# Kernel tuning notes

Measured on AMD Instinct MI355X. Metric: run time of the kernel, lower is better.

Reference implementation:

```python
import math
import jax, jax.numpy as jnp
import numpy as np

H, W = 24, 24
N = H * W
D = 1024
B = 32
MAX_ITERS = 6

# 9 relative neighbor offsets (3x3 window, row-major)
_REL = np.array([[-1, -1], [-1, 0], [-1, 1], [0, -1], [0, 0], [0, 1], [1, -1], [1, 0], [1, 1]])


def _neighbor_cols():
    y, x = np.meshgrid(np.arange(H), np.arange(W), indexing='ij')
    ny = np.clip(y[None] + _REL[:, 0, None, None], 0, H - 1)  # [9,H,W]
    nx = np.clip(x[None] + _REL[:, 1, None, None], 0, W - 1)
    return jnp.asarray((ny * W + nx).reshape(9, N))  # [9,N]


def setup_inputs() -> dict:
    key = jax.random.key(0)
    ks = jax.random.split(key, 8)
    return {
        'tok2d': jax.random.normal(ks[0], (B, N + 1, D), dtype=jnp.float32),
        'dw_w': jax.random.normal(ks[1], (D, 1, 3, 3), dtype=jnp.float32) * 0.02,
        'pw_w': jax.random.normal(ks[2], (9, D, 1, 1), dtype=jnp.float32) * 0.02,
        'pw_b': jnp.zeros((9,), dtype=jnp.float32),
        'q_w': jax.random.normal(ks[3], (D, D), dtype=jnp.float32) * 0.02,
        'q_b': jax.random.normal(ks[4], (D,), dtype=jnp.float32) * 0.02,
        'v_w': jax.random.normal(ks[5], (D, D), dtype=jnp.float32) * 0.02,
        'v_b': jax.random.normal(ks[6], (D,), dtype=jnp.float32) * 0.02,
        'K': 256,
        'MAX_TOKENS': 128,
    }


def _affinity_head(patch2d, dw_w, pw_w, pw_b):
    # patch2d: [B,H,W,D] -> Q: [B,H,W,9]
    x = jnp.transpose(patch2d, (0, 3, 1, 2))  # NCHW
    x = jax.lax.conv_general_dilated(
        x, dw_w, window_strides=(1, 1), padding='SAME',
        feature_group_count=D,
        dimension_numbers=('NCHW', 'OIHW', 'NCHW'))
    x = jnp.einsum('bdhw,od->bohw', x, pw_w[:, :, 0, 0]) + pw_b[None, :, None, None]
    return jax.nn.softmax(jnp.transpose(x, (0, 2, 3, 1)), axis=-1)


def _build_token_affinity(Q):
    # Q: [B,H,W,9] -> A: [B,N,N] via 9 shifted-neighbor scatters
    cols = _neighbor_cols()                                   # [9,N]
    rows = jnp.broadcast_to(jnp.arange(N)[None, :], (9, N))   # [9,N]
    vals = jnp.moveaxis(Q.reshape(-1, N, 9), -1, 1).reshape(-1, 9 * N)  # [B,9*N]
    A = jnp.zeros((Q.shape[0], N, N), dtype=Q.dtype)
    return A.at[:, rows.reshape(-1), cols.reshape(-1)].add(vals)


def _cluster_roots(A):
    roots = jnp.argmax(A, axis=-1)  # [B,N]
    for _ in range(MAX_ITERS):      # pointer jumping (idempotent once converged)
        roots = jnp.take_along_axis(roots, roots, axis=1)
    return roots


def _cluster_centers(E, roots, K):
    b = E.shape[0]
    bidx = jnp.arange(b)[:, None]
    centers_sum = jnp.zeros_like(E).at[bidx, roots].add(E)          # [B,N,D]
    counts = jnp.zeros(E.shape[:2], E.dtype).at[bidx, roots].add(1.0)  # [B,N]
    _, topk_idx = jax.lax.top_k(counts, K)
    ord_idx = jnp.sort(topk_idx, axis=1)
    cs = jnp.take_along_axis(centers_sum, ord_idx[:, :, None], axis=1)
    cnt = jnp.take_along_axis(counts, ord_idx, axis=1)
    C = cs / jnp.clip(cnt, 1.0, None)[:, :, None]
    return C, cnt


def reference(tok2d, dw_w, pw_w, pw_b, q_w, q_b, v_w, v_b, K, MAX_TOKENS):
    cls_tok = tok2d[:, :1, :]                 # [B,1,D]
    patch = tok2d[:, 1:, :]                   # [B,N,D]
    Q = _affinity_head(patch.reshape(-1, H, W, D), dw_w, pw_w, pw_b)
    A = _build_token_affinity(Q)
    roots = _cluster_roots(A)
    C, cnt = _cluster_centers(patch, roots, K)
    Q_cls = cls_tok @ q_w.T + q_b             # [B,1,D]
    K_v = C @ v_w.T + v_b                     # [B,K,D]
    scores = jnp.einsum('bod,bkd->bk', Q_cls, K_v) / math.sqrt(D)
    valid = jnp.where(cnt > 0, scores, -jnp.inf)
    m = min(MAX_TOKENS, C.shape[1])
    _, idx = jax.lax.top_k(valid, m)
    idx_sorted = jnp.sort(idx, axis=-1)
    return jnp.take_along_axis(C, idx_sorted[:, :, None], axis=1)  # [B,m,D]
```

## Files before the change

kernel.cpp:

```cpp
#include <hip/hip_runtime.h>
#include <math.h>

#define Hh 24
#define Ww 24
#define Nn 576
#define Dd 1024
#define Bb 32
#define Kk 256
#define Mm 128
#define TOKSTRIDE (577 * 1024)

#define R0_OFF 0
#define MEMB_OFF 1152
#define OFFS_OFF 1728
#define ORD_OFF 2304
#define CNT_OFF 2560
#define P_OFF 2944
#define QC_OFF 3776
#define U_OFF 4800
#define T_OFF 5824
#define UP_OFF 6144

__device__ __forceinline__ float* batch_base(float* out, int b) {
  return out + (size_t)b * Mm * Dd;
}

__device__ __forceinline__ float wave_sum_dpp(float x) {
  int y;
  y = __builtin_amdgcn_update_dpp(0, __float_as_int(x), 0x111, 0xf, 0xf, true);
  x += __int_as_float(y);
  y = __builtin_amdgcn_update_dpp(0, __float_as_int(x), 0x112, 0xf, 0xf, true);
  x += __int_as_float(y);
  y = __builtin_amdgcn_update_dpp(0, __float_as_int(x), 0x114, 0xf, 0xf, true);
  x += __int_as_float(y);
  y = __builtin_amdgcn_update_dpp(0, __float_as_int(x), 0x118, 0xf, 0xf, true);
  x += __int_as_float(y);
  y = __builtin_amdgcn_update_dpp(0, __float_as_int(x), 0x142, 0xa, 0xf, true);
  x += __int_as_float(y);
  y = __builtin_amdgcn_update_dpp(0, __float_as_int(x), 0x143, 0xc, 0xf, true);
  x += __int_as_float(y);
  return x;
}

__device__ __forceinline__ float row_sum_dpp(float x) {
  int y;
  y = __builtin_amdgcn_update_dpp(0, __float_as_int(x), 0x111, 0xf, 0xf, true);
  x += __int_as_float(y);
  y = __builtin_amdgcn_update_dpp(0, __float_as_int(x), 0x112, 0xf, 0xf, true);
  x += __int_as_float(y);
  y = __builtin_amdgcn_update_dpp(0, __float_as_int(x), 0x114, 0xf, 0xf, true);
  x += __int_as_float(y);
  y = __builtin_amdgcn_update_dpp(0, __float_as_int(x), 0x118, 0xf, 0xf, true);
  x += __int_as_float(y);
  return x;
}

__global__ __launch_bounds__(256) void qcls_kernel(
    const float* __restrict__ tok2d, const float* __restrict__ q_w,
    const float* __restrict__ q_b, float* __restrict__ outb) {
  int dp = blockIdx.x;
  int wave = threadIdx.x >> 6;
  int lane = threadIdx.x & 63;
  float4 qv[4];
#pragma unroll
  for (int i = 0; i < 4; i++)
    qv[i] = *(const float4*)(q_w + (size_t)dp * Dd + lane * 4 + 256 * i);
  float qb = q_b[dp];
  for (int bb = 0; bb < 8; bb++) {
    int b = wave * 8 + bb;
    const float* cls = tok2d + (size_t)b * TOKSTRIDE;
    float a = 0.f;
#pragma unroll
    for (int i = 0; i < 4; i++) {
      float4 cv = *(const float4*)(cls + lane * 4 + 256 * i);
      a += qv[i].x * cv.x + qv[i].y * cv.y + qv[i].z * cv.z + qv[i].w * cv.w;
    }
    a = wave_sum_dpp(a);
    if (lane == 63) batch_base(outb, b)[QC_OFF + dp] = a + qb;
  }
}

__global__ __launch_bounds__(256) void u_part_kernel(const float* __restrict__ v_w,
                                                     float* __restrict__ outb) {
  int b = blockIdx.x >> 3;
  int chunk = blockIdx.x & 7;
  int tid = threadIdx.x;
  int d0 = tid * 4;
  float* basef = batch_base(outb, b);
  __shared__ float qs[128];
  if (tid < 128) qs[tid] = basef[QC_OFF + chunk * 128 + tid];
  __syncthreads();
  float4 a = make_float4(0.f, 0.f, 0.f, 0.f);
#pragma unroll 4
  for (int dpl = 0; dpl < 128; dpl++) {
    int dp = chunk * 128 + dpl;
    float4 vv = *(const float4*)(v_w + (size_t)dp * Dd + d0);
    float qq = qs[dpl];
    a.x += qq * vv.x; a.y += qq * vv.y; a.z += qq * vv.z; a.w += qq * vv.w;
  }
  *(float4*)(basef + UP_OFF + chunk * Dd + d0) = a;
}

__global__ __launch_bounds__(256) void combine_ut_kernel(
    const float* __restrict__ v_b, float* __restrict__ outb) {
  int b = blockIdx.x;
  int tid = threadIdx.x;
  float* basef = batch_base(outb, b);
  int d0 = tid * 4;
  float4 s = make_float4(0.f, 0.f, 0.f, 0.f);
#pragma unroll
  for (int c = 0; c < 8; c++) {
    float4 v = *(const float4*)(basef + UP_OFF + c * Dd + d0);
    s.x += v.x; s.y += v.y; s.z += v.z; s.w += v.w;
  }
  *(float4*)(basef + U_OFF + d0) = s;

  float a = 0.f;
  for (int i = tid; i < Dd; i += 256) a += basef[QC_OFF + i] * v_b[i];
  __shared__ float sh[256];
  sh[tid] = a;
  __syncthreads();
  for (int st = 128; st > 0; st >>= 1) {
    if (tid < st) sh[tid] += sh[tid + st];
    __syncthreads();
  }
  if (tid == 0) basef[T_OFF] = sh[0];
}

__global__ __launch_bounds__(256, 4) void affinity_p_root_kernel(
    const float* __restrict__ tok2d, const float* __restrict__ dw_w,
    const float* __restrict__ pw_w, const float* __restrict__ pw_b,
    float* __restrict__ outb) {
  int wave = threadIdx.x >> 6;
  int lane = threadIdx.x & 63;
  int blk = (blockIdx.x & 7) * (Bb * Hh * 3 / 8) + (blockIdx.x >> 3);
  int b = blk / (Hh * 3);
  int rem = blk % (Hh * 3);
  int y = rem / 3;
  int x0 = (rem % 3) * 8;
  int d0 = wave * 256 + lane * 4;
  const float* patch = tok2d + (size_t)b * TOKSTRIDE + Dd;
  float* basef = batch_base(outb, b);

  __shared__ float red[8 * 167 + 8];

  union { float4 v[9]; float f[36]; } w;
  const float4* dwp = (const float4*)(dw_w + (size_t)d0 * 9);
#pragma unroll
  for (int j = 0; j < 9; j++) w.v[j] = dwp[j];
  float4 u4 = *(const float4*)(basef + U_OFF + d0);

  float4 cc[8];
  float pacc[8];
#pragma unroll
  for (int t = 0; t < 8; t++) {
    cc[t] = make_float4(0.f, 0.f, 0.f, 0.f);
    pacc[t] = 0.f;
  }
#pragma unroll
  for (int ky = 0; ky < 3; ky++) {
    int yy = y + ky - 1;
    if (yy < 0 || yy >= Hh) continue;
    const float* prow = patch + (size_t)(yy * Ww) * Dd + d0;
    float4 wA = make_float4(0.f, 0.f, 0.f, 0.f);
    if (x0 > 0) wA = *(const float4*)(prow + (size_t)(x0 - 1) * Dd);
    float4 wB = *(const float4*)(prow + (size_t)x0 * Dd);
    int kA = ky * 3, kB = ky * 3 + 1, kC = ky * 3 + 2;
#pragma unroll
    for (int t = 0; t < 8; t++) {
      float4 wC = make_float4(0.f, 0.f, 0.f, 0.f);
      int xx = x0 + t + 1;
      if (xx < Ww) wC = *(const float4*)(prow + (size_t)xx * Dd);
      cc[t].x += wA.x * w.f[kA] + wB.x * w.f[kB] + wC.x * w.f[kC];
      cc[t].y += wA.y * w.f[9 + kA] + wB.y * w.f[9 + kB] + wC.y * w.f[9 + kC];
      cc[t].z += wA.z * w.f[18 + kA] + wB.z * w.f[18 + kB] + wC.z * w.f[18 + kC];
      cc[t].w += wA.w * w.f[27 + kA] + wB.w * w.f[27 + kB] + wC.w * w.f[27 + kC];
      if (ky == 1)
        pacc[t] = wB.x * u4.x + wB.y * u4.y + wB.z * u4.z + wB.w * u4.w;
      wA = wB;
      wB = wC;
    }
  }

  __builtin_amdgcn_sched_barrier(0);

  float4 pw[9];
#pragma unroll
  for (int o = 0; o < 9; o++)
    pw[o] = *(const float4*)(pw_w + (size_t)o * Dd + d0);

#pragma unroll
  for (int t = 0; t < 8; t++) {
    float acc[10];
#pragma unroll
    for (int o = 0; o < 9; o++) {
      acc[o] = cc[t].x * pw[o].x + cc[t].y * pw[o].y + cc[t].z * pw[o].z +
               cc[t].w * pw[o].w;
    }
    acc[9] = pacc[t];
#pragma unroll
    for (int o = 0; o < 10; o++) acc[o] = row_sum_dpp(acc[o]);
    if ((lane & 15) == 15) {
      int r = wave * 4 + (lane >> 4);
#pragma unroll
      for (int o = 0; o < 10; o++) red[t * 167 + r * 10 + o] = acc[o];
    }
  }
  __syncthreads();

  if (lane < 2) {
    int t = wave * 2 + lane;
    int x = x0 + t;
    int n = y * Ww + x;
    float l[10];
#pragma unroll
    for (int o = 0; o < 10; o++) l[o] = 0.f;
    for (int r = 0; r < 16; r++) {
#pragma unroll
      for (int o = 0; o < 10; o++) l[o] += red[t * 167 + r * 10 + o];
    }
    float q[9];
    float mx = -INFINITY;
#pragma unroll
    for (int o = 0; o < 9; o++) {
      l[o] += pw_b[o];
      mx = fmaxf(mx, l[o]);
    }
    float ssum = 0.f;
#pragma unroll
    for (int o = 0; o < 9; o++) {
      q[o] = expf(l[o] - mx);
      ssum += q[o];
    }
#pragma unroll
    for (int o = 0; o < 9; o++) q[o] = q[o] / ssum;

    int colv[9];
#pragma unroll
    for (int o = 0; o < 9; o++) {
      int dy = o / 3 - 1, dx = o % 3 - 1;
      int ny = min(max(y + dy, 0), Hh - 1);
      int nx = min(max(x + dx, 0), Ww - 1);
      colv[o] = ny * Ww + nx;
    }
    float best = -1.f;
    int bcol = 1 << 30;
#pragma unroll
    for (int o = 0; o < 9; o++) {
      float v = 0.f;
#pragma unroll
      for (int oo = 0; oo < 9; oo++)
        v = (colv[oo] == colv[o]) ? v + q[oo] : v;
      if (v > best || (v == best && colv[o] < bcol)) {
        best = v;
        bcol = colv[o];
      }
    }
    ((int*)basef)[R0_OFF + n] = bcol;
    basef[P_OFF + n] = l[9];
  }
}

__global__ __launch_bounds__(576) void cluster_topk_kernel(float* __restrict__ outb) {
  int b = blockIdx.x;
  int n = threadIdx.x;
  int* base = (int*)batch_base(outb, b);
  __shared__ int ra[Nn], rb[Nn], scnt[Nn], soff[Nn];
  ra[n] = base[R0_OFF + n];
  scnt[n] = 0;
  __syncthreads();
  for (int it = 0; it < 6; it++) {
    rb[n] = ra[ra[n]];
    __syncthreads();
    ra[n] = rb[n];
    __syncthreads();
  }
  int r = ra[n];
  atomicAdd(&scnt[r], 1);
  __syncthreads();

  soff[n] = scnt[n];
  __syncthreads();
  for (int s = 1; s < Nn; s <<= 1) {
    int v = (n >= s) ? soff[n - s] : 0;
    __syncthreads();
    soff[n] += v;
    __syncthreads();
  }
  int excl = soff[n] - scnt[n];
  base[OFFS_OFF + n] = excl;
  int offr = soff[r] - scnt[r];
  int rk = 0;
  for (int m = 0; m < n; m++) rk += (ra[m] == r);
  base[MEMB_OFF + offr + rk] = n;

  int cn = scnt[n];
  int rank = 0;
  for (int m = 0; m < Nn; m++) {
    int cm = scnt[m];
    rank += (cm > cn) || (cm == cn && m < n);
  }
  int sl = (rank < Kk) ? 1 : 0;
  rb[n] = sl;
  __syncthreads();
  for (int s = 1; s < Nn; s <<= 1) {
    int v = (n >= s) ? rb[n - s] : 0;
    __syncthreads();
    rb[n] += v;
    __syncthreads();
  }
  if (sl) {
    int pos = rb[n] - 1;
    base[ORD_OFF + pos] = n;
    base[CNT_OFF + pos] = cn;
  }
}

__global__ __launch_bounds__(256) void scores_plan_kernel(float* __restrict__ outb) {
  int b = blockIdx.x;
  int tid = threadIdx.x;
  int wave = tid >> 6, lane = tid & 63;
  float* basef = batch_base(outb, b);
  int* base = (int*)basef;
  __shared__ int s_mem[Nn], s_off[Nn], s_ord[Kk], s_cnt[Kk], s_out[Mm];
  __shared__ float ss[Kk];
  __shared__ int sel[Kk];
  for (int i = tid; i < Nn; i += 256) {
    s_mem[i] = base[MEMB_OFF + i];
    s_off[i] = base[OFFS_OFF + i];
  }
  s_ord[tid] = base[ORD_OFF + tid];
  s_cnt[tid] = base[CNT_OFF + tid];
  float tt = basef[T_OFF];
  __syncthreads();

  int idx = s_ord[tid];
  int c = s_cnt[tid];
  float s;
  if (c > 0) {
    int off = s_off[idx];
    float sum = 0.f;
    for (int j = 0; j < c; j++) sum += basef[P_OFF + s_mem[off + j]];
    s = (sum / (float)c + tt) * (1.0f / 32.0f);
  } else {
    s = -INFINITY;
  }
  ss[tid] = s;
  __syncthreads();

  float vk = ss[tid];
  int rank = 0;
  for (int m = 0; m < Kk; m++) {
    float vm = ss[m];
    rank += (vm > vk) || (vm == vk && m < tid);
  }
  sel[tid] = (rank < Mm) ? 1 : 0;
  __syncthreads();
  if (sel[tid]) {
    int pos = 0;
    for (int m = 0; m < tid; m++) pos += sel[m];
    s_out[pos] = tid;
  }
  __syncthreads();

  for (int kp = wave; kp < Mm; kp += 4) {
    int k = s_out[kp];
    int kidx = s_ord[k];
    int kc = s_cnt[k];
    int koff = s_off[kidx];
    int* row = base + kp * Dd;
    if (lane == 0) row[0] = kc;
    for (int j = lane; j < kc; j += 64) row[1 + j] = s_mem[koff + j];
  }
}

__global__ __launch_bounds__(256) void output_kernel(
    const float* __restrict__ tok2d, float* __restrict__ outb) {
  int blk = blockIdx.x;
  int b = blk / Mm;
  int tid = threadIdx.x;
  float* rowf = outb + (size_t)blk * Dd;
  int* rowi = (int*)rowf;
  __shared__ int s_c;
  __shared__ int s_m[Nn];
  if (tid == 0) s_c = rowi[0];
  __syncthreads();
  int c = s_c;
  for (int j = tid; j < c; j += 256) s_m[j] = rowi[1 + j];
  __syncthreads();
  const float* patch = tok2d + (size_t)b * TOKSTRIDE + Dd;
  int d0 = tid * 4;
  float4 acc = make_float4(0.f, 0.f, 0.f, 0.f);
  for (int j = 0; j < c; j++) {
    float4 rv = *(const float4*)(patch + (size_t)s_m[j] * Dd + d0);
    acc.x += rv.x; acc.y += rv.y; acc.z += rv.z; acc.w += rv.w;
  }
  float inv = 1.0f / (float)max(c, 1);
  *(float4*)(rowf + d0) =
      make_float4(acc.x * inv, acc.y * inv, acc.z * inv, acc.w * inv);
}

extern "C" void kernel_launch(void* const* d_in, const int* in_sizes, int n_in,
                              void* d_out, int out_size, void* d_ws,
                              size_t ws_size, hipStream_t stream) {
  const float* tok2d = (const float*)d_in[0];
  const float* dw_w = (const float*)d_in[1];
  const float* pw_w = (const float*)d_in[2];
  const float* pw_b = (const float*)d_in[3];
  const float* q_w = (const float*)d_in[4];
  const float* q_b = (const float*)d_in[5];
  const float* v_w = (const float*)d_in[6];
  const float* v_b = (const float*)d_in[7];
  float* out = (float*)d_out;
  (void)d_ws; (void)ws_size;

  qcls_kernel<<<dim3(Dd), dim3(256), 0, stream>>>(tok2d, q_w, q_b, out);
  u_part_kernel<<<dim3(Bb * 8), dim3(256), 0, stream>>>(v_w, out);
  combine_ut_kernel<<<dim3(Bb), dim3(256), 0, stream>>>(v_b, out);
  affinity_p_root_kernel<<<dim3(Bb * Hh * 3), dim3(256), 0, stream>>>(
      tok2d, dw_w, pw_w, pw_b, out);
  cluster_topk_kernel<<<dim3(Bb), dim3(Nn), 0, stream>>>(out);
  scores_plan_kernel<<<dim3(Bb), dim3(256), 0, stream>>>(out);
  output_kernel<<<dim3(Bb * Mm), dim3(256), 0, stream>>>(tok2d, out);
}
```

Before: 246.1 us.

## Fuse u/t computation and cluster+scores kernels, reduce register pressure in affinity

Merges the split-K u_part and combine kernels into one u_t kernel that handles 4 batches per block over the full D reduction, and merges cluster_topk and scores_plan into a single kernel that keeps membership, offsets and P values in shared memory instead of round-tripping through global memory. The affinity kernel now reduces and stores the P partial immediately instead of keeping 8 accumulators live, and raises the occupancy hint to 8 blocks. This cuts two kernel launches and global traffic. The cost is that the u_t kernel runs only 32 blocks, each doing a long serial loop over v_w, which may underuse the GPU.

```diff
diff --git a/kernel.cpp b/kernel.cpp
--- a/kernel.cpp
+++ b/kernel.cpp
@@ -11,15 +11,10 @@
 #define TOKSTRIDE (577 * 1024)
 
 #define R0_OFF 0
-#define MEMB_OFF 1152
-#define OFFS_OFF 1728
-#define ORD_OFF 2304
-#define CNT_OFF 2560
 #define P_OFF 2944
 #define QC_OFF 3776
 #define U_OFF 4800
 #define T_OFF 5824
-#define UP_OFF 6144
 
 __device__ __forceinline__ float* batch_base(float* out, int b) {
   return out + (size_t)b * Mm * Dd;
@@ -80,54 +75,39 @@
   }
 }
 
-__global__ __launch_bounds__(256) void u_part_kernel(const float* __restrict__ v_w,
-                                                     float* __restrict__ outb) {
-  int b = blockIdx.x >> 3;
-  int chunk = blockIdx.x & 7;
-  int tid = threadIdx.x;
-  int d0 = tid * 4;
-  float* basef = batch_base(outb, b);
-  __shared__ float qs[128];
-  if (tid < 128) qs[tid] = basef[QC_OFF + chunk * 128 + tid];
+__global__ __launch_bounds__(256) void u_t_kernel(const float* __restrict__ v_w,
+                                                  const float* __restrict__ v_b,
+                                                  float* __restrict__ outb) {
+  int bg = blockIdx.x >> 2;
+  int ds = blockIdx.x & 3;
+  int bi = threadIdx.x >> 6;
+  int col = threadIdx.x & 63;
+  int b = bg * 4 + bi;
+  int d0 = ds * 256 + col * 4;
+  __shared__ float qs[4][Dd];
+  for (int i = threadIdx.x; i < 4 * Dd; i += 256) {
+    int bb = i >> 10;
+    qs[bb][i & 1023] = batch_base(outb, bg * 4 + bb)[QC_OFF + (i & 1023)];
+  }
   __syncthreads();
   float4 a = make_float4(0.f, 0.f, 0.f, 0.f);
 #pragma unroll 4
-  for (int dpl = 0; dpl < 128; dpl++) {
-    int dp = chunk * 128 + dpl;
+  for (int dp = 0; dp < Dd; dp++) {
     float4 vv = *(const float4*)(v_w + (size_t)dp * Dd + d0);
-    float qq = qs[dpl];
+    float qq = qs[bi][dp];
     a.x += qq * vv.x; a.y += qq * vv.y; a.z += qq * vv.z; a.w += qq * vv.w;
   }
-  *(float4*)(basef + UP_OFF + chunk * Dd + d0) = a;
-}
-
-__global__ __launch_bounds__(256) void combine_ut_kernel(
-    const float* __restrict__ v_b, float* __restrict__ outb) {
-  int b = blockIdx.x;
-  int tid = threadIdx.x;
-  float* basef = batch_base(outb, b);
-  int d0 = tid * 4;
-  float4 s = make_float4(0.f, 0.f, 0.f, 0.f);
-#pragma unroll
-  for (int c = 0; c < 8; c++) {
-    float4 v = *(const float4*)(basef + UP_OFF + c * Dd + d0);
-    s.x += v.x; s.y += v.y; s.z += v.z; s.w += v.w;
-  }
-  *(float4*)(basef + U_OFF + d0) = s;
-
-  float a = 0.f;
-  for (int i = tid; i < Dd; i += 256) a += basef[QC_OFF + i] * v_b[i];
-  __shared__ float sh[256];
-  sh[tid] = a;
-  __syncthreads();
-  for (int st = 128; st > 0; st >>= 1) {
-    if (tid < st) sh[tid] += sh[tid + st];
-    __syncthreads();
-  }
-  if (tid == 0) basef[T_OFF] = sh[0];
-}
-
-__global__ __launch_bounds__(256, 4) void affinity_p_root_kernel(
+  *(float4*)(batch_base(outb, b) + U_OFF + d0) = a;
+
+  if (ds == 0) {
+    float s = 0.f;
+    for (int i = col; i < Dd; i += 64) s += qs[bi][i] * v_b[i];
+    s = wave_sum_dpp(s);
+    if (col == 63) batch_base(outb, b)[T_OFF] = s;
+  }
+}
+
+__global__ __launch_bounds__(256, 8) void affinity_p_root_kernel(
     const float* __restrict__ tok2d, const float* __restrict__ dw_w,
     const float* __restrict__ pw_w, const float* __restrict__ pw_b,
     float* __restrict__ outb) {
@@ -151,12 +131,8 @@
   float4 u4 = *(const float4*)(basef + U_OFF + d0);
 
   float4 cc[8];
-  float pacc[8];
-#pragma unroll
-  for (int t = 0; t < 8; t++) {
-    cc[t] = make_float4(0.f, 0.f, 0.f, 0.f);
-    pacc[t] = 0.f;
-  }
+#pragma unroll
+  for (int t = 0; t < 8; t++) cc[t] = make_float4(0.f, 0.f, 0.f, 0.f);
 #pragma unroll
   for (int ky = 0; ky < 3; ky++) {
     int yy = y + ky - 1;
@@ -175,8 +151,12 @@
       cc[t].y += wA.y * w.f[9 + kA] + wB.y * w.f[9 + kB] + wC.y * w.f[9 + kC];
       cc[t].z += wA.z * w.f[18 + kA] + wB.z * w.f[18 + kB] + wC.z * w.f[18 + kC];
       cc[t].w += wA.w * w.f[27 + kA] + wB.w * w.f[27 + kB] + wC.w * w.f[27 + kC];
-      if (ky == 1)
-        pacc[t] = wB.x * u4.x + wB.y * u4.y + wB.z * u4.z + wB.w * u4.w;
+      if (ky == 1) {
+        float pa = wB.x * u4.x + wB.y * u4.y + wB.z * u4.z + wB.w * u4.w;
+        pa = row_sum_dpp(pa);
+        if ((lane & 15) == 15)
+          red[t * 167 + (wave * 4 + (lane >> 4)) * 10 + 9] = pa;
+      }
       wA = wB;
       wB = wC;
     }
@@ -191,19 +171,18 @@
 
 #pragma unroll
   for (int t = 0; t < 8; t++) {
-    float acc[10];
+    float acc[9];
 #pragma unroll
     for (int o = 0; o < 9; o++) {
       acc[o] = cc[t].x * pw[o].x + cc[t].y * pw[o].y + cc[t].z * pw[o].z +
                cc[t].w * pw[o].w;
     }
-    acc[9] = pacc[t];
-#pragma unroll
-    for (int o = 0; o < 10; o++) acc[o] = row_sum_dpp(acc[o]);
+#pragma unroll
+    for (int o = 0; o < 9; o++) acc[o] = row_sum_dpp(acc[o]);
     if ((lane & 15) == 15) {
       int r = wave * 4 + (lane >> 4);
 #pragma unroll
-      for (int o = 0; o < 10; o++) red[t * 167 + r * 10 + o] = acc[o];
+      for (int o = 0; o < 9; o++) red[t * 167 + r * 10 + o] = acc[o];
     }
   }
   __syncthreads();
@@ -261,12 +240,18 @@
   }
 }
 
-__global__ __launch_bounds__(576) void cluster_topk_kernel(float* __restrict__ outb) {
+__global__ __launch_bounds__(576) void cluster_scores_plan_kernel(
+    float* __restrict__ outb) {
   int b = blockIdx.x;
   int n = threadIdx.x;
-  int* base = (int*)batch_base(outb, b);
-  __shared__ int ra[Nn], rb[Nn], scnt[Nn], soff[Nn];
+  float* basef = batch_base(outb, b);
+  int* base = (int*)basef;
+  __shared__ int ra[Nn], rb[Nn], scnt[Nn], soff[Nn], smem[Nn];
+  __shared__ float sp[Nn];
+  __shared__ int s_ord[Kk], s_cnt[Kk], sel[Kk], s_out[Mm];
+  __shared__ float ss[Kk];
   ra[n] = base[R0_OFF + n];
+  sp[n] = basef[P_OFF + n];
   scnt[n] = 0;
   __syncthreads();
   for (int it = 0; it < 6; it++) {
@@ -287,12 +272,10 @@
     soff[n] += v;
     __syncthreads();
   }
-  int excl = soff[n] - scnt[n];
-  base[OFFS_OFF + n] = excl;
   int offr = soff[r] - scnt[r];
   int rk = 0;
   for (int m = 0; m < n; m++) rk += (ra[m] == r);
-  base[MEMB_OFF + offr + rk] = n;
+  smem[offr + rk] = n;
 
   int cn = scnt[n];
   int rank = 0;
@@ -311,66 +294,53 @@
   }
   if (sl) {
     int pos = rb[n] - 1;
-    base[ORD_OFF + pos] = n;
-    base[CNT_OFF + pos] = cn;
-  }
-}
-
-__global__ __launch_bounds__(256) void scores_plan_kernel(float* __restrict__ outb) {
-  int b = blockIdx.x;
-  int tid = threadIdx.x;
-  int wave = tid >> 6, lane = tid & 63;
-  float* basef = batch_base(outb, b);
-  int* base = (int*)basef;
-  __shared__ int s_mem[Nn], s_off[Nn], s_ord[Kk], s_cnt[Kk], s_out[Mm];
-  __shared__ float ss[Kk];
-  __shared__ int sel[Kk];
-  for (int i = tid; i < Nn; i += 256) {
-    s_mem[i] = base[MEMB_OFF + i];
-    s_off[i] = base[OFFS_OFF + i];
-  }
-  s_ord[tid] = base[ORD_OFF + tid];
-  s_cnt[tid] = base[CNT_OFF + tid];
-  float tt = basef[T_OFF];
-  __syncthreads();
-
-  int idx = s_ord[tid];
-  int c = s_cnt[tid];
-  float s;
-  if (c > 0) {
-    int off = s_off[idx];
-    float sum = 0.f;
-    for (int j = 0; j < c; j++) sum += basef[P_OFF + s_mem[off + j]];
-    s = (sum / (float)c + tt) * (1.0f / 32.0f);
-  } else {
-    s = -INFINITY;
-  }
-  ss[tid] = s;
-  __syncthreads();
-
-  float vk = ss[tid];
-  int rank = 0;
-  for (int m = 0; m < Kk; m++) {
-    float vm = ss[m];
-    rank += (vm > vk) || (vm == vk && m < tid);
-  }
-  sel[tid] = (rank < Mm) ? 1 : 0;
-  __syncthreads();
-  if (sel[tid]) {
+    s_ord[pos] = n;
+    s_cnt[pos] = cn;
+  }
+  __syncthreads();
+
+  if (n < Kk) {
+    int idx = s_ord[n];
+    int c = s_cnt[n];
+    float s;
+    if (c > 0) {
+      int off = soff[idx] - scnt[idx];
+      float sum = 0.f;
+      for (int j = 0; j < c; j++) sum += sp[smem[off + j]];
+      s = (sum / (float)c + basef[T_OFF]) * (1.0f / 32.0f);
+    } else {
+      s = -INFINITY;
+    }
+    ss[n] = s;
+  }
+  __syncthreads();
+
+  if (n < Kk) {
+    float vk = ss[n];
+    int rank2 = 0;
+    for (int m = 0; m < Kk; m++) {
+      float vm = ss[m];
+      rank2 += (vm > vk) || (vm == vk && m < n);
+    }
+    sel[n] = (rank2 < Mm) ? 1 : 0;
+  }
+  __syncthreads();
+  if (n < Kk && sel[n]) {
     int pos = 0;
-    for (int m = 0; m < tid; m++) pos += sel[m];
-    s_out[pos] = tid;
-  }
-  __syncthreads();
-
-  for (int kp = wave; kp < Mm; kp += 4) {
+    for (int m = 0; m < n; m++) pos += sel[m];
+    s_out[pos] = n;
+  }
+  __syncthreads();
+
+  int w9 = n >> 6, lane = n & 63;
+  for (int kp = w9; kp < Mm; kp += 9) {
     int k = s_out[kp];
     int kidx = s_ord[k];
     int kc = s_cnt[k];
-    int koff = s_off[kidx];
+    int koff = soff[kidx] - scnt[kidx];
     int* row = base + kp * Dd;
     if (lane == 0) row[0] = kc;
-    for (int j = lane; j < kc; j += 64) row[1 + j] = s_mem[koff + j];
+    for (int j = lane; j < kc; j += 64) row[1 + j] = smem[koff + j];
   }
 }
 
@@ -415,11 +385,9 @@
   (void)d_ws; (void)ws_size;
 
   qcls_kernel<<<dim3(Dd), dim3(256), 0, stream>>>(tok2d, q_w, q_b, out);
-  u_part_kernel<<<dim3(Bb * 8), dim3(256), 0, stream>>>(v_w, out);
-  combine_ut_kernel<<<dim3(Bb), dim3(256), 0, stream>>>(v_b, out);
+  u_t_kernel<<<dim3(32), dim3(256), 0, stream>>>(v_w, v_b, out);
   affinity_p_root_kernel<<<dim3(Bb * Hh * 3), dim3(256), 0, stream>>>(
       tok2d, dw_w, pw_w, pw_b, out);
-  cluster_topk_kernel<<<dim3(Bb), dim3(Nn), 0, stream>>>(out);
-  scores_plan_kernel<<<dim3(Bb), dim3(256), 0, stream>>>(out);
+  cluster_scores_plan_kernel<<<dim3(Bb), dim3(Nn), 0, stream>>>(out);
   output_kernel<<<dim3(Bb * Mm), dim3(256), 0, stream>>>(tok2d, out);
 }
```

New measurement: 524.1 us. 2.13x slower.
